# Performance work log

Measured on AMD Instinct MI355X. Metric: run time of the kernel, lower is better.

## Reference

```python
import jax, jax.numpy as jnp
import numpy as np

B, N, CIN, H, W = 4, 1024, 256, 256, 256
R, C = 32, 32            # N = R*C table grid cells
PH, PW, SR = 3, 3, 2     # pool_size, sampling_ratio
D = 512                  # out_channels
SCALE = 0.25             # spatial_scale: image coords -> feature coords
IMG = 1024.0             # image size (H/SCALE)


def setup_inputs() -> dict:
    key = jax.random.key(0)
    ks = jax.random.split(key, 12)
    feats = jax.random.normal(ks[0], (B, CIN, H, W), jnp.float32)
    # build valid quadrilateral boxes (axis-aligned rectangles as 8-pt polys)
    x1 = jax.random.uniform(ks[1], (B, N), minval=0.0, maxval=IMG - 130.0)
    y1 = jax.random.uniform(ks[2], (B, N), minval=0.0, maxval=IMG - 130.0)
    bw = jax.random.uniform(ks[3], (B, N), minval=16.0, maxval=128.0)
    bh = jax.random.uniform(ks[4], (B, N), minval=16.0, maxval=128.0)
    x2, y2 = x1 + bw, y1 + bh
    boxes = jnp.stack([x1, y1, x2, y1, x2, y2, x1, y2], axis=-1)  # [B,N,8]
    img_sizes = jnp.full((B, 2), IMG, jnp.float32)
    IN = CIN * PH * PW
    W1 = jax.random.normal(ks[5], (IN, D), jnp.float32) * 0.02
    b1 = jnp.zeros((D,), jnp.float32)
    W2 = jax.random.normal(ks[6], (D, D), jnp.float32) * 0.02
    b2 = jnp.zeros((D,), jnp.float32)
    Wb = jax.random.normal(ks[7], (4, D), jnp.float32) * 0.02
    bb = jnp.zeros((D,), jnp.float32)
    g1 = jnp.ones((D,), jnp.float32); be1 = jnp.zeros((D,), jnp.float32)
    g2 = jnp.ones((D,), jnp.float32); be2 = jnp.zeros((D,), jnp.float32)
    return {"feats": feats, "boxes": boxes, "img_sizes": img_sizes,
            "W1": W1, "b1": b1, "W2": W2, "b2": b2, "Wb": Wb, "bb": bb,
            "g1": g1, "be1": be1, "g2": g2, "be2": be2}


def _layer_norm(x, g, b, eps=1e-5):
    mu = jnp.mean(x, axis=-1, keepdims=True)
    var = jnp.mean(jnp.square(x - mu), axis=-1, keepdims=True)
    return (x - mu) * jax.lax.rsqrt(var + eps) * g + b


def _bilinear(img, ys, xs):
    # img [Cin,H,W]; ys,xs [P] -> [Cin,P]; torchvision roi_align semantics:
    # zero outside (-1, dim); clamp into [0, dim-1] before interpolation.
    h, w = img.shape[1], img.shape[2]
    valid = (ys > -1.0) & (ys < h) & (xs > -1.0) & (xs < w)
    y = jnp.clip(ys, 0.0, h - 1.0)
    x = jnp.clip(xs, 0.0, w - 1.0)
    y0 = jnp.floor(y).astype(jnp.int32); x0 = jnp.floor(x).astype(jnp.int32)
    y1 = jnp.minimum(y0 + 1, h - 1);     x1 = jnp.minimum(x0 + 1, w - 1)
    ly = y - y0; lx = x - x0; hy = 1.0 - ly; hx = 1.0 - lx
    v = (img[:, y0, x0] * (hy * hx) + img[:, y0, x1] * (hy * lx)
         + img[:, y1, x0] * (ly * hx) + img[:, y1, x1] * (ly * lx))
    return v * valid


def _roi_align_one(img, bb):
    # img [Cin,H,W]; bb [N,4] already in feature coords -> [N,Cin,PH,PW]
    x1, y1, x2, y2 = bb[:, 0], bb[:, 1], bb[:, 2], bb[:, 3]
    rw = jnp.maximum(x2 - x1, 1.0); rh = jnp.maximum(y2 - y1, 1.0)
    binw = rw / PW; binh = rh / PH
    off = (jnp.arange(SR, dtype=jnp.float32) + 0.5) / SR
    gy = (jnp.arange(PH, dtype=jnp.float32)[:, None] + off[None, :]).reshape(-1)  # [PH*SR]
    gx = (jnp.arange(PW, dtype=jnp.float32)[:, None] + off[None, :]).reshape(-1)  # [PW*SR]
    ys = y1[:, None] + gy[None, :] * binh[:, None]  # [N,PH*SR]
    xs = x1[:, None] + gx[None, :] * binw[:, None]  # [N,PW*SR]
    YY = jnp.broadcast_to(ys[:, :, None], (bb.shape[0], PH * SR, PW * SR)).reshape(-1)
    XX = jnp.broadcast_to(xs[:, None, :], (bb.shape[0], PH * SR, PW * SR)).reshape(-1)
    vals = _bilinear(img, YY, XX)  # [Cin, N*PH*SR*PW*SR]
    vals = vals.reshape(CIN, bb.shape[0], PH, SR, PW, SR).mean(axis=(3, 5))
    return vals.transpose(1, 0, 2, 3)


def reference(feats, boxes, img_sizes, W1, b1, W2, b2, Wb, bb, g1, be1, g2, be2):
    # poly2bbox: [B,N,8] -> [B,N,4] axis-aligned boxes
    px, py = boxes[..., 0::2], boxes[..., 1::2]
    bbox = jnp.stack([px.min(-1), py.min(-1), px.max(-1), py.max(-1)], axis=-1)
    # rotated/regular RoIAlign (here bbox path), vmapped over batch images
    pooled = jax.vmap(_roi_align_one)(feats, bbox * SCALE)     # [B,N,Cin,PH,PW]
    flat = pooled.reshape(B, N, CIN * PH * PW)
    lines_feat = jax.nn.relu(flat @ W1 + b1) @ W2 + b2          # [B,N,D]
    # bbox positional embedding (coords normalized by image size)
    denom = jnp.concatenate([img_sizes, img_sizes], axis=-1)[:, None, :]  # [B,1,4] (w,h,w,h)
    pos = _layer_norm(bbox / denom @ Wb + bb, g1, be1)
    out = _layer_norm(lines_feat + pos, g2, be2)                # [B,N,D]
    # align_cells_feat: pack cells into grid [B,D,R,C] (uniform grid -> no pad)
    aligned = out.transpose(0, 2, 1).reshape(B, D, R, C)
    masks = jnp.ones((B, R, C), jnp.float32)
    return aligned, masks
```

## Files before the change

### kernel.cpp

```cpp
#include <hip/hip_runtime.h>
#include <hip/hip_bf16.h>
#include <cstdint>
#include <cstddef>

#define B_    4
#define N_    1024
#define CIN_  256
#define HW_   256
#define D_    512
#define INK_  2304
#define BN_   4096

typedef __attribute__((ext_vector_type(8))) short bf16x8;
typedef __attribute__((ext_vector_type(4))) float f32x4;
typedef __attribute__((ext_vector_type(4))) unsigned short us4;

__device__ __forceinline__ unsigned short f2bf(float f) {
    union { float f; unsigned u; } v; v.f = f;
    unsigned r = v.u + 0x7fffu + ((v.u >> 16) & 1u);
    return (unsigned short)(r >> 16);
}

template <typename OutT>
__global__ __launch_bounds__(256) void k_t64(
    const float* __restrict__ src, OutT* __restrict__ dst,
    int Mrows, int Ncols, size_t sBatch, size_t dBatch)
{
    constexpr int PAD = (sizeof(OutT) == 2) ? 66 : 67;
    __shared__ OutT tile[64][PAD];
    const int n0 = blockIdx.x * 64;
    const int m0 = blockIdx.y * 64;
    const float* s = src + (size_t)blockIdx.z * sBatch;
    OutT* d = dst + (size_t)blockIdx.z * dBatch;
    const int t  = threadIdx.x;
    const int rr = t >> 4;
    const int cc = t & 15;

    #pragma unroll
    for (int i = 0; i < 4; ++i) {
        int row = i * 16 + rr;
        float4 v = *(const float4*)(s + (size_t)(m0 + row) * Ncols + n0 + cc * 4);
        if constexpr (sizeof(OutT) == 2) {
            tile[row][cc * 4 + 0] = f2bf(v.x);
            tile[row][cc * 4 + 1] = f2bf(v.y);
            tile[row][cc * 4 + 2] = f2bf(v.z);
            tile[row][cc * 4 + 3] = f2bf(v.w);
        } else {
            tile[row][cc * 4 + 0] = v.x;
            tile[row][cc * 4 + 1] = v.y;
            tile[row][cc * 4 + 2] = v.z;
            tile[row][cc * 4 + 3] = v.w;
        }
    }
    __syncthreads();
    #pragma unroll
    for (int i = 0; i < 4; ++i) {
        int p = i * 16 + rr;
        OutT v0 = tile[cc * 4 + 0][p];
        OutT v1 = tile[cc * 4 + 1][p];
        OutT v2 = tile[cc * 4 + 2][p];
        OutT v3 = tile[cc * 4 + 3][p];
        OutT* dp = d + (size_t)(n0 + p) * Mrows + m0 + cc * 4;
        if constexpr (sizeof(OutT) == 2) {
            *(us4*)dp = (us4){(unsigned short)v0, (unsigned short)v1,
                              (unsigned short)v2, (unsigned short)v3};
        } else {
            *(float4*)dp = make_float4(v0, v1, v2, v3);
        }
    }
}

__global__ __launch_bounds__(256) void k_roi2(
    const unsigned short* __restrict__ featsT, const float* __restrict__ boxes,
    unsigned short* __restrict__ flat)
{
    __shared__ int   so[2][36][4];
    __shared__ float sw[2][36][4];
    const int t = threadIdx.x;

    if (t < 72) {
        const int mbx = t / 36, s = t % 36;
        const int mbn = blockIdx.x * 2 + mbx;
        const float* bx = boxes + (size_t)mbn * 8;
        float xmn = fminf(fminf(bx[0], bx[2]), fminf(bx[4], bx[6]));
        float xmx = fmaxf(fmaxf(bx[0], bx[2]), fmaxf(bx[4], bx[6]));
        float ymn = fminf(fminf(bx[1], bx[3]), fminf(bx[5], bx[7]));
        float ymx = fmaxf(fmaxf(bx[1], bx[3]), fmaxf(bx[5], bx[7]));
        float sx1 = xmn * 0.25f, sy1 = ymn * 0.25f;
        float sx2 = xmx * 0.25f, sy2 = ymx * 0.25f;
        float rw = fmaxf(sx2 - sx1, 1.0f), rh = fmaxf(sy2 - sy1, 1.0f);
        float binw = rw * (1.0f / 3.0f), binh = rh * (1.0f / 3.0f);
        int row = s / 6, col = s % 6;
        float y = sy1 + (row * 0.5f + 0.25f) * binh;
        float x = sx1 + (col * 0.5f + 0.25f) * binw;
        float valid = (y > -1.0f && y < 256.0f && x > -1.0f && x < 256.0f) ? 1.0f : 0.0f;
        y = fminf(fmaxf(y, 0.0f), 255.0f);
        x = fminf(fmaxf(x, 0.0f), 255.0f);
        int y0 = (int)floorf(y), x0 = (int)floorf(x);
        int y1 = min(y0 + 1, 255), x1 = min(x0 + 1, 255);
        float ly = y - (float)y0, lx = x - (float)x0;
        float hy = 1.0f - ly, hx = 1.0f - lx;
        float m = 0.25f * valid;
        so[mbx][s][0] = y0 * HW_ + x0;  so[mbx][s][1] = y0 * HW_ + x1;
        so[mbx][s][2] = y1 * HW_ + x0;  so[mbx][s][3] = y1 * HW_ + x1;
        sw[mbx][s][0] = hy * hx * m;    sw[mbx][s][1] = hy * lx * m;
        sw[mbx][s][2] = ly * hx * m;    sw[mbx][s][3] = ly * lx * m;
    }
    __syncthreads();

    const int bxi = t >> 7;
    const int tid = t & 127;
    const int bn  = blockIdx.x * 2 + bxi;
    const int b   = bn >> 10;
    const unsigned* basep = (const unsigned*)featsT + (size_t)b * (65536u * 128u) + tid;

    float a0[9] = {0,0,0,0,0,0,0,0,0};
    float a1[9] = {0,0,0,0,0,0,0,0,0};
    #pragma unroll
    for (int j = 0; j < 36; ++j) {
        const int bin = ((j / 6) >> 1) * 3 + ((j % 6) >> 1);
        int o0 = so[bxi][j][0], o1 = so[bxi][j][1], o2 = so[bxi][j][2], o3 = so[bxi][j][3];
        float w0 = sw[bxi][j][0], w1 = sw[bxi][j][1], w2 = sw[bxi][j][2], w3 = sw[bxi][j][3];
        unsigned u0 = basep[(size_t)o0 << 7];
        unsigned u1 = basep[(size_t)o1 << 7];
        unsigned u2 = basep[(size_t)o2 << 7];
        unsigned u3 = basep[(size_t)o3 << 7];
        float lo = w0 * __uint_as_float(u0 << 16) + w1 * __uint_as_float(u1 << 16)
                 + w2 * __uint_as_float(u2 << 16) + w3 * __uint_as_float(u3 << 16);
        float hi = w0 * __uint_as_float(u0 & 0xffff0000u) + w1 * __uint_as_float(u1 & 0xffff0000u)
                 + w2 * __uint_as_float(u2 & 0xffff0000u) + w3 * __uint_as_float(u3 & 0xffff0000u);
        a0[bin] += lo;
        a1[bin] += hi;
    }

    unsigned short tmp[18];
    #pragma unroll
    for (int k = 0; k < 9; ++k) { tmp[k] = f2bf(a0[k]); tmp[9 + k] = f2bf(a1[k]); }
    unsigned* dst = (unsigned*)(flat + (size_t)bn * INK_ + tid * 18);
    #pragma unroll
    for (int k = 0; k < 9; ++k) dst[k] = (unsigned)tmp[2 * k] | ((unsigned)tmp[2 * k + 1] << 16);
}

__global__ __launch_bounds__(256) void k_convert(
    const float* __restrict__ W1, const float* __restrict__ W2,
    unsigned short* __restrict__ W1t, unsigned short* __restrict__ W2t)
{
    int i = blockIdx.x * 256 + threadIdx.x;
    const int n1 = INK_ * D_;
    if (i < n1) {
        int n = i / INK_, k = i % INK_;
        W1t[i] = f2bf(W1[(size_t)k * D_ + n]);
    } else {
        int j = i - n1;
        if (j < D_ * D_) {
            int n = j / D_, k = j % D_;
            W2t[j] = f2bf(W2[(size_t)k * D_ + n]);
        }
    }
}

__global__ __launch_bounds__(256) void k_roi(
    const float* __restrict__ feats, const float* __restrict__ boxes,
    unsigned short* __restrict__ flat)
{
    __shared__ int   so[36][4];
    __shared__ float sw[36][4];
    const int bn = blockIdx.x;
    const int b  = bn >> 10;
    const int t  = threadIdx.x;

    if (t < 36) {
        const float* bx = boxes + (size_t)bn * 8;
        float xmn = fminf(fminf(bx[0], bx[2]), fminf(bx[4], bx[6]));
        float xmx = fmaxf(fmaxf(bx[0], bx[2]), fmaxf(bx[4], bx[6]));
        float ymn = fminf(fminf(bx[1], bx[3]), fminf(bx[5], bx[7]));
        float ymx = fmaxf(fmaxf(bx[1], bx[3]), fmaxf(bx[5], bx[7]));
        float sx1 = xmn * 0.25f, sy1 = ymn * 0.25f;
        float sx2 = xmx * 0.25f, sy2 = ymx * 0.25f;
        float rw = fmaxf(sx2 - sx1, 1.0f), rh = fmaxf(sy2 - sy1, 1.0f);
        float binw = rw * (1.0f / 3.0f), binh = rh * (1.0f / 3.0f);
        int row = t / 6, col = t % 6;
        float y = sy1 + (row * 0.5f + 0.25f) * binh;
        float x = sx1 + (col * 0.5f + 0.25f) * binw;
        float valid = (y > -1.0f && y < 256.0f && x > -1.0f && x < 256.0f) ? 1.0f : 0.0f;
        y = fminf(fmaxf(y, 0.0f), 255.0f);
        x = fminf(fmaxf(x, 0.0f), 255.0f);
        int y0 = (int)floorf(y), x0 = (int)floorf(x);
        int y1 = min(y0 + 1, 255), x1 = min(x0 + 1, 255);
        float ly = y - (float)y0, lx = x - (float)x0;
        float hy = 1.0f - ly, hx = 1.0f - lx;
        float m = 0.25f * valid;
        so[t][0] = y0 * HW_ + x0;  so[t][1] = y0 * HW_ + x1;
        so[t][2] = y1 * HW_ + x0;  so[t][3] = y1 * HW_ + x1;
        sw[t][0] = hy * hx * m;    sw[t][1] = hy * lx * m;
        sw[t][2] = ly * hx * m;    sw[t][3] = ly * lx * m;
    }
    __syncthreads();

    const float* base = feats + ((size_t)(b * CIN_ + t) << 16);
    float acc[9] = {0.f,0.f,0.f,0.f,0.f,0.f,0.f,0.f,0.f};
    #pragma unroll
    for (int j = 0; j < 36; ++j) {
        const int bin = ((j / 6) >> 1) * 3 + ((j % 6) >> 1);
        float v = sw[j][0] * base[so[j][0]] + sw[j][1] * base[so[j][1]]
                + sw[j][2] * base[so[j][2]] + sw[j][3] * base[so[j][3]];
        acc[bin] += v;
    }
    unsigned short* dst = flat + (size_t)bn * INK_ + t * 9;
    #pragma unroll
    for (int k = 0; k < 9; ++k) dst[k] = f2bf(acc[k]);
}

template <int K, bool RELU_BF16OUT>
__global__ __launch_bounds__(256) void k_gemm(
    const unsigned short* __restrict__ A,
    const unsigned short* __restrict__ Bt,
    const float* __restrict__ bias,
    unsigned short* __restrict__ Cbf,
    float* __restrict__ Cf)
{
    __shared__ __align__(16) unsigned short Asl[64 * 40];
    __shared__ __align__(16) unsigned short Bsl[64 * 40];

    const int t  = threadIdx.x;
    const int m0 = blockIdx.x * 64;
    const int n0 = blockIdx.y * 64;
    const int w  = t >> 6;
    const int l  = t & 63;
    const int lane16 = l & 15;
    const int q  = l >> 4;

    f32x4 acc[4] = {};

    const int srow = t >> 2;
    const int sch  = t & 3;
    const unsigned short* ga = A  + (size_t)(m0 + srow) * K + sch * 8;
    const unsigned short* gb = Bt + (size_t)(n0 + srow) * K + sch * 8;
    unsigned short* la = &Asl[srow * 40 + sch * 8];
    unsigned short* lb = &Bsl[srow * 40 + sch * 8];

    for (int k0 = 0; k0 < K; k0 += 32) {
        __syncthreads();
        *(bf16x8*)la = *(const bf16x8*)(ga + k0);
        *(bf16x8*)lb = *(const bf16x8*)(gb + k0);
        __syncthreads();
        bf16x8 af = *(const bf16x8*)&Asl[(w * 16 + lane16) * 40 + q * 8];
        #pragma unroll
        for (int nt = 0; nt < 4; ++nt) {
            bf16x8 bfv = *(const bf16x8*)&Bsl[(nt * 16 + lane16) * 40 + q * 8];
            acc[nt] = __builtin_amdgcn_mfma_f32_16x16x32_bf16(af, bfv, acc[nt], 0, 0, 0);
        }
    }

    #pragma unroll
    for (int nt = 0; nt < 4; ++nt) {
        int col = n0 + nt * 16 + lane16;
        float bs = bias[col];
        #pragma unroll
        for (int r = 0; r < 4; ++r) {
            int rowg = m0 + w * 16 + q * 4 + r;
            float v = acc[nt][r] + bs;
            if constexpr (RELU_BF16OUT) {
                v = fmaxf(v, 0.0f);
                Cbf[(size_t)rowg * D_ + col] = f2bf(v);
            } else {
                Cf[(size_t)rowg * D_ + col] = v;
            }
        }
    }
}

__device__ __forceinline__ void breduce2(float& a, float& b, float* red, int t) {
    #pragma unroll
    for (int off = 32; off > 0; off >>= 1) {
        a += __shfl_down(a, off);
        b += __shfl_down(b, off);
    }
    int w = t >> 6;
    if ((t & 63) == 0) { red[w] = a; red[4 + w] = b; }
    __syncthreads();
    a = red[0] + red[1] + red[2] + red[3];
    b = red[4] + red[5] + red[6] + red[7];
    __syncthreads();
}

template <bool DIRECT>
__global__ __launch_bounds__(256) void k_tail(
    const float* __restrict__ lines, const float* __restrict__ boxes,
    const float* __restrict__ img_sizes,
    const float* __restrict__ Wb,  const float* __restrict__ bbv,
    const float* __restrict__ g1,  const float* __restrict__ be1,
    const float* __restrict__ g2,  const float* __restrict__ be2,
    float* __restrict__ out)
{
    __shared__ float red[8];
    const int row = blockIdx.x;
    const int b = row >> 10, n = row & 1023;
    const int t = threadIdx.x;

    const float* bx = boxes + (size_t)row * 8;
    float xmn = fminf(fminf(bx[0], bx[2]), fminf(bx[4], bx[6]));
    float xmx = fmaxf(fmaxf(bx[0], bx[2]), fmaxf(bx[4], bx[6]));
    float ymn = fminf(fminf(bx[1], bx[3]), fminf(bx[5], bx[7]));
    float ymx = fmaxf(fmaxf(bx[1], bx[3]), fmaxf(bx[5], bx[7]));
    float s0 = img_sizes[b * 2], s1 = img_sizes[b * 2 + 1];
    float q0 = xmn / s0, q1 = ymn / s1, q2 = xmx / s0, q3 = ymx / s1;

    float tv[2], sv[2];
    float sum = 0.f, sumsq = 0.f;
    #pragma unroll
    for (int i = 0; i < 2; ++i) {
        int d = t + i * 256;
        float v = q0 * Wb[d] + q1 * Wb[512 + d] + q2 * Wb[1024 + d] + q3 * Wb[1536 + d] + bbv[d];
        tv[i] = v; sum += v; sumsq += v * v;
    }
    breduce2(sum, sumsq, red, t);
    float mu = sum * (1.0f / 512.0f);
    float var = sumsq * (1.0f / 512.0f) - mu * mu;
    float rs = rsqrtf(var + 1e-5f);

    sum = 0.f; sumsq = 0.f;
    #pragma unroll
    for (int i = 0; i < 2; ++i) {
        int d = t + i * 256;
        float p = (tv[i] - mu) * rs * g1[d] + be1[d];
        float s = lines[(size_t)row * D_ + d] + p;
        sv[i] = s; sum += s; sumsq += s * s;
    }
    breduce2(sum, sumsq, red, t);
    float mu2 = sum * (1.0f / 512.0f);
    float var2 = sumsq * (1.0f / 512.0f) - mu2 * mu2;
    float rs2 = rsqrtf(var2 + 1e-5f);

    #pragma unroll
    for (int i = 0; i < 2; ++i) {
        int d = t + i * 256;
        float o = (sv[i] - mu2) * rs2 * g2[d] + be2[d];
        if constexpr (DIRECT)
            out[(size_t)b * (D_ * N_) + (size_t)d * N_ + n] = o;
        else
            out[(size_t)row * D_ + d] = o;
    }
}

__global__ __launch_bounds__(256) void k_mask(float* __restrict__ out) {
    int i = blockIdx.x * 256 + threadIdx.x;
    if (i < B_ * 32 * 32) out[(size_t)B_ * D_ * N_ + i] = 1.0f;
}

extern "C" void kernel_launch(void* const* d_in, const int* in_sizes, int n_in,
                              void* d_out, int out_size, void* d_ws, size_t ws_size,
                              hipStream_t stream)
{
    const float* feats = (const float*)d_in[0];
    const float* boxes = (const float*)d_in[1];
    const float* img   = (const float*)d_in[2];
    const float* W1    = (const float*)d_in[3];
    const float* b1    = (const float*)d_in[4];
    const float* W2    = (const float*)d_in[5];
    const float* b2    = (const float*)d_in[6];
    const float* Wb    = (const float*)d_in[7];
    const float* bbv   = (const float*)d_in[8];
    const float* g1    = (const float*)d_in[9];
    const float* be1   = (const float*)d_in[10];
    const float* g2    = (const float*)d_in[11];
    const float* be2   = (const float*)d_in[12];
    float* out = (float*)d_out;
    char* ws = (char*)d_ws;

    const size_t OFF_FEATST = 0;
    const size_t OFF_W1T    = 134217728;
    const size_t OFF_W2T    = 136577024;
    const size_t OFF_FLAT   = 137101312;
    const size_t OFF_ACT    = 155975680;
    const size_t OFF_LINES  = 160169984;
    const size_t OFF_OROW   = 168558592;
    const size_t NEED       = 176947200;

    if (ws_size >= NEED) {
        unsigned short* featsT = (unsigned short*)(ws + OFF_FEATST);
        unsigned short* W1t    = (unsigned short*)(ws + OFF_W1T);
        unsigned short* W2t    = (unsigned short*)(ws + OFF_W2T);
        unsigned short* flat   = (unsigned short*)(ws + OFF_FLAT);
        unsigned short* act    = (unsigned short*)(ws + OFF_ACT);
        float*          lines  = (float*)(ws + OFF_LINES);
        float*          orow   = (float*)(ws + OFF_OROW);

        k_t64<unsigned short><<<dim3(HW_*HW_/64, CIN_/64, B_), 256, 0, stream>>>(
            feats, featsT, CIN_, HW_*HW_, (size_t)CIN_*HW_*HW_, (size_t)CIN_*HW_*HW_);
        k_t64<unsigned short><<<dim3(D_/64, INK_/64, 1), 256, 0, stream>>>(
            W1, W1t, INK_, D_, 0, 0);
        k_t64<unsigned short><<<dim3(D_/64, D_/64, 1), 256, 0, stream>>>(
            W2, W2t, D_, D_, 0, 0);

        k_roi2<<<BN_/2, 256, 0, stream>>>(featsT, boxes, flat);

        dim3 gg(64, 8);
        k_gemm<INK_, true ><<<gg, 256, 0, stream>>>(flat, W1t, b1, act, nullptr);
        k_gemm<D_,   false><<<gg, 256, 0, stream>>>(act,  W2t, b2, nullptr, lines);

        k_tail<false><<<BN_, 256, 0, stream>>>(lines, boxes, img, Wb, bbv, g1, be1, g2, be2, orow);
        k_t64<float><<<dim3(D_/64, N_/64, B_), 256, 0, stream>>>(
            orow, out, N_, D_, (size_t)N_*D_, (size_t)D_*N_);
        k_mask<<<16, 256, 0, stream>>>(out);
    } else {
        unsigned short* W1t  = (unsigned short*)(ws);
        unsigned short* W2t  = (unsigned short*)(ws + 2359296);
        unsigned short* flat = (unsigned short*)(ws + 2883584);
        unsigned short* act  = (unsigned short*)(ws + 21757952);
        float*          lines= (float*)(ws + 25952256);

        const int convTotal = INK_ * D_ + D_ * D_;
        k_convert<<<(convTotal + 255) / 256, 256, 0, stream>>>(W1, W2, W1t, W2t);
        k_roi<<<BN_, 256, 0, stream>>>(feats, boxes, flat);
        dim3 gg(64, 8);
        k_gemm<INK_, true ><<<gg, 256, 0, stream>>>(flat, W1t, b1, act, nullptr);
        k_gemm<D_,   false><<<gg, 256, 0, stream>>>(act,  W2t, b2, nullptr, lines);
        k_tail<true><<<BN_, 256, 0, stream>>>(lines, boxes, img, Wb, bbv, g1, be1, g2, be2, out);
        k_mask<<<16, 256, 0, stream>>>(out);
    }
}
```

Before: 510.6 us.

## Widen ROI gather loads and add double-buffered LDS-DMA GEMM

The ROI-align gather kernel now handles four boxes per block, and each thread loads 8 bytes (four bf16 channels) per sample point instead of 4. This halves the number of gather instructions. The GEMMs are replaced with a 128x64-tile kernel that uses global_load_lds to stream A/B tiles into double-buffered shared memory while MFMA runs on the previous tile. This should raise arithmetic reuse and overlap loads with compute, at the cost of possible LDS bank conflicts and fewer blocks in the grid.

After: 506.4 us. No clear change (-0.8%).

```diff
diff --git a/kernel.cpp b/kernel.cpp
--- a/kernel.cpp
+++ b/kernel.cpp
@@ -14,6 +14,9 @@
 typedef __attribute__((ext_vector_type(8))) short bf16x8;
 typedef __attribute__((ext_vector_type(4))) float f32x4;
 typedef __attribute__((ext_vector_type(4))) unsigned short us4;
+
+#define AS1(p) ((const __attribute__((address_space(1))) void*)(p))
+#define AS3(p) ((__attribute__((address_space(3))) void*)(p))
 
 __device__ __forceinline__ unsigned short f2bf(float f) {
     union { float f; unsigned u; } v; v.f = f;
@@ -70,17 +73,17 @@
     }
 }
 
-__global__ __launch_bounds__(256) void k_roi2(
+__global__ __launch_bounds__(256) void k_roi3(
     const unsigned short* __restrict__ featsT, const float* __restrict__ boxes,
     unsigned short* __restrict__ flat)
 {
-    __shared__ int   so[2][36][4];
-    __shared__ float sw[2][36][4];
+    __shared__ int   so[4][36][4];
+    __shared__ float sw[4][36][4];
     const int t = threadIdx.x;
 
-    if (t < 72) {
-        const int mbx = t / 36, s = t % 36;
-        const int mbn = blockIdx.x * 2 + mbx;
+    if (t < 144) {
+        const int mbx = t / 36, s = t - mbx * 36;
+        const int mbn = blockIdx.x * 4 + mbx;
         const float* bx = boxes + (size_t)mbn * 8;
         float xmn = fminf(fminf(bx[0], bx[2]), fminf(bx[4], bx[6]));
         float xmx = fmaxf(fmaxf(bx[0], bx[2]), fmaxf(bx[4], bx[6]));
@@ -108,37 +111,112 @@
     }
     __syncthreads();
 
-    const int bxi = t >> 7;
-    const int tid = t & 127;
-    const int bn  = blockIdx.x * 2 + bxi;
+    const int bxi = t >> 6;
+    const int tid = t & 63;
+    const int bn  = blockIdx.x * 4 + bxi;
     const int b   = bn >> 10;
-    const unsigned* basep = (const unsigned*)featsT + (size_t)b * (65536u * 128u) + tid;
+    const uint2* basep = (const uint2*)featsT + (size_t)b * (65536ull * 64ull) + tid;
 
     float a0[9] = {0,0,0,0,0,0,0,0,0};
     float a1[9] = {0,0,0,0,0,0,0,0,0};
+    float a2[9] = {0,0,0,0,0,0,0,0,0};
+    float a3[9] = {0,0,0,0,0,0,0,0,0};
     #pragma unroll
     for (int j = 0; j < 36; ++j) {
         const int bin = ((j / 6) >> 1) * 3 + ((j % 6) >> 1);
-        int o0 = so[bxi][j][0], o1 = so[bxi][j][1], o2 = so[bxi][j][2], o3 = so[bxi][j][3];
-        float w0 = sw[bxi][j][0], w1 = sw[bxi][j][1], w2 = sw[bxi][j][2], w3 = sw[bxi][j][3];
-        unsigned u0 = basep[(size_t)o0 << 7];
-        unsigned u1 = basep[(size_t)o1 << 7];
-        unsigned u2 = basep[(size_t)o2 << 7];
-        unsigned u3 = basep[(size_t)o3 << 7];
-        float lo = w0 * __uint_as_float(u0 << 16) + w1 * __uint_as_float(u1 << 16)
-                 + w2 * __uint_as_float(u2 << 16) + w3 * __uint_as_float(u3 << 16);
-        float hi = w0 * __uint_as_float(u0 & 0xffff0000u) + w1 * __uint_as_float(u1 & 0xffff0000u)
-                 + w2 * __uint_as_float(u2 & 0xffff0000u) + w3 * __uint_as_float(u3 & 0xffff0000u);
-        a0[bin] += lo;
-        a1[bin] += hi;
-    }
-
-    unsigned short tmp[18];
-    #pragma unroll
-    for (int k = 0; k < 9; ++k) { tmp[k] = f2bf(a0[k]); tmp[9 + k] = f2bf(a1[k]); }
-    unsigned* dst = (unsigned*)(flat + (size_t)bn * INK_ + tid * 18);
-    #pragma unroll
-    for (int k = 0; k < 9; ++k) dst[k] = (unsigned)tmp[2 * k] | ((unsigned)tmp[2 * k + 1] << 16);
+        #pragma unroll
+        for (int p = 0; p < 4; ++p) {
+            float wgt = sw[bxi][j][p];
+            uint2 u = basep[(size_t)so[bxi][j][p] << 6];
+            a0[bin] += wgt * __uint_as_float(u.x << 16);
+            a1[bin] += wgt * __uint_as_float(u.x & 0xffff0000u);
+            a2[bin] += wgt * __uint_as_float(u.y << 16);
+            a3[bin] += wgt * __uint_as_float(u.y & 0xffff0000u);
+        }
+    }
+
+    unsigned short tmp[36];
+    #pragma unroll
+    for (int k = 0; k < 9; ++k) {
+        tmp[k] = f2bf(a0[k]); tmp[9 + k] = f2bf(a1[k]);
+        tmp[18 + k] = f2bf(a2[k]); tmp[27 + k] = f2bf(a3[k]);
+    }
+    unsigned* dst = (unsigned*)(flat + (size_t)bn * INK_ + tid * 36);
+    #pragma unroll
+    for (int k = 0; k < 18; ++k)
+        dst[k] = (unsigned)tmp[2 * k] | ((unsigned)tmp[2 * k + 1] << 16);
+}
+
+template <int K, bool RELU_BF16OUT>
+__global__ __launch_bounds__(256) void k_gemmB(
+    const unsigned short* __restrict__ A,
+    const unsigned short* __restrict__ Bt,
+    const float* __restrict__ bias,
+    unsigned short* __restrict__ Cbf,
+    float* __restrict__ Cf)
+{
+    __shared__ __align__(16) unsigned short As[2][128 * 32];
+    __shared__ __align__(16) unsigned short Bs[2][64 * 32];
+
+    const int t = threadIdx.x;
+    const int w = t >> 6;
+    const int lane = t & 63;
+    const int lane16 = lane & 15;
+    const int q = lane >> 4;
+    const int m0 = blockIdx.x * 128;
+    const int n0 = blockIdx.y * 64;
+
+    const int r4 = lane >> 2, c4 = lane & 3;
+    const unsigned short* gA0 = A + (size_t)(m0 + w * 16 + r4) * K + c4 * 8;
+    const unsigned short* gA1 = gA0 + (size_t)64 * K;
+    const unsigned short* gB  = Bt + (size_t)(n0 + w * 16 + r4) * K + c4 * 8;
+
+    f32x4 acc[2][4] = {};
+
+    __builtin_amdgcn_global_load_lds(AS1(gA0), AS3(&As[0][(w * 16) * 32]), 16, 0, 0);
+    __builtin_amdgcn_global_load_lds(AS1(gA1), AS3(&As[0][(64 + w * 16) * 32]), 16, 0, 0);
+    __builtin_amdgcn_global_load_lds(AS1(gB ), AS3(&Bs[0][(w * 16) * 32]), 16, 0, 0);
+    gA0 += 32; gA1 += 32; gB += 32;
+
+    int cur = 0;
+    for (int k0 = 0; k0 < K; k0 += 32) {
+        __syncthreads();
+        if (k0 + 32 < K) {
+            __builtin_amdgcn_global_load_lds(AS1(gA0), AS3(&As[cur ^ 1][(w * 16) * 32]), 16, 0, 0);
+            __builtin_amdgcn_global_load_lds(AS1(gA1), AS3(&As[cur ^ 1][(64 + w * 16) * 32]), 16, 0, 0);
+            __builtin_amdgcn_global_load_lds(AS1(gB ), AS3(&Bs[cur ^ 1][(w * 16) * 32]), 16, 0, 0);
+            gA0 += 32; gA1 += 32; gB += 32;
+        }
+        bf16x8 a0 = *(const bf16x8*)&As[cur][(w * 32 + lane16) * 32 + q * 8];
+        bf16x8 a1 = *(const bf16x8*)&As[cur][(w * 32 + 16 + lane16) * 32 + q * 8];
+        #pragma unroll
+        for (int nt = 0; nt < 4; ++nt) {
+            bf16x8 bv = *(const bf16x8*)&Bs[cur][(nt * 16 + lane16) * 32 + q * 8];
+            acc[0][nt] = __builtin_amdgcn_mfma_f32_16x16x32_bf16(a0, bv, acc[0][nt], 0, 0, 0);
+            acc[1][nt] = __builtin_amdgcn_mfma_f32_16x16x32_bf16(a1, bv, acc[1][nt], 0, 0, 0);
+        }
+        cur ^= 1;
+    }
+
+    #pragma unroll
+    for (int nt = 0; nt < 4; ++nt) {
+        int col = n0 + nt * 16 + lane16;
+        float bs = bias[col];
+        #pragma unroll
+        for (int mg = 0; mg < 2; ++mg) {
+            #pragma unroll
+            for (int r = 0; r < 4; ++r) {
+                int row = m0 + w * 32 + mg * 16 + q * 4 + r;
+                float v = acc[mg][nt][r] + bs;
+                if constexpr (RELU_BF16OUT) {
+                    v = fmaxf(v, 0.0f);
+                    Cbf[(size_t)row * D_ + col] = f2bf(v);
+                } else {
+                    Cf[(size_t)row * D_ + col] = v;
+                }
+            }
+        }
+    }
 }
 
 __global__ __launch_bounds__(256) void k_convert(
@@ -393,11 +471,11 @@
         k_t64<unsigned short><<<dim3(D_/64, D_/64, 1), 256, 0, stream>>>(
             W2, W2t, D_, D_, 0, 0);
 
-        k_roi2<<<BN_/2, 256, 0, stream>>>(featsT, boxes, flat);
-
-        dim3 gg(64, 8);
-        k_gemm<INK_, true ><<<gg, 256, 0, stream>>>(flat, W1t, b1, act, nullptr);
-        k_gemm<D_,   false><<<gg, 256, 0, stream>>>(act,  W2t, b2, nullptr, lines);
+        k_roi3<<<BN_/4, 256, 0, stream>>>(featsT, boxes, flat);
+
+        dim3 gg(32, 8);
+        k_gemmB<INK_, true ><<<gg, 256, 0, stream>>>(flat, W1t, b1, act, nullptr);
+        k_gemmB<D_,   false><<<gg, 256, 0, stream>>>(act,  W2t, b2, nullptr, lines);
 
         k_tail<false><<<BN_, 256, 0, stream>>>(lines, boxes, img, Wb, bbv, g1, be1, g2, be2, orow);
         k_t64<float><<<dim3(D_/64, N_/64, B_), 256, 0, stream>>>(
```
